# Optimization experiments

Hardware: AMD Instinct MI355X
Metric: run time of the kernel (lower is better)

Reference implementation:

```python
import jax, jax.numpy as jnp
import numpy as np

N = 50000   # nodes
E = 640000  # edges
IN = 256    # in_dim
H = 128     # hidden
OUT = 40    # out_dim
EPS = 1e-5  # BatchNorm eps


def setup_inputs() -> dict:
    key = jax.random.key(0)
    ks = jax.random.split(key, 14)
    x = jax.random.normal(ks[0], (N, IN), jnp.float32)
    edge_index = jax.random.randint(ks[1], (2, E), 0, N)
    def lin(k, fan_in, shape):
        return jax.random.normal(k, shape, jnp.float32) / np.float32(np.sqrt(fan_in))
    return {
        "x": x,
        "edge_index": edge_index,
        # block 0 (256 -> 128, has res_proj)
        "W0": lin(ks[2], IN, (IN, H)),
        "b0": jnp.zeros((H,), jnp.float32),
        "g0": jnp.ones((H,), jnp.float32),
        "be0": jnp.zeros((H,), jnp.float32),
        "pW": lin(ks[3], IN, (IN, H)),
        "pb": jnp.zeros((H,), jnp.float32),
        # block 1 (128 -> 128, identity residual)
        "W1": lin(ks[4], H, (H, H)),
        "b1": jnp.zeros((H,), jnp.float32),
        "g1": jnp.ones((H,), jnp.float32),
        "be1": jnp.zeros((H,), jnp.float32),
        # head
        "hW": lin(ks[5], H, (H, OUT)),
        "hb": jnp.zeros((OUT,), jnp.float32),
    }


def _gcn_conv(x, W, b, edge_index):
    """GCNConv(improved=True): x' = D^-1/2 (A + 2I) D^-1/2 (x W) + b."""
    h = x @ W  # [N, dout]
    row, col = edge_index[0], edge_index[1]  # source -> target
    # degree of A + 2I (edge_weight = 1, self-loop fill = 2.0)
    deg = jnp.zeros((N,), h.dtype).at[col].add(1.0) + 2.0
    dis = jax.lax.rsqrt(deg)  # deg > 0 always (self-loops)
    norm = dis[row] * dis[col]  # [E]
    # neighbor aggregation: scatter-add normalized messages to targets
    agg = jnp.zeros_like(h).at[col].add(norm[:, None] * h[row])
    # self-loop contribution with weight 2.0
    agg = agg + (2.0 * dis * dis)[:, None] * h
    return agg + b


def _bn(x, gamma, beta):
    # batch statistics (training-mode BatchNorm math), biased variance
    m = jnp.mean(x, axis=0)
    v = jnp.mean(jnp.square(x - m), axis=0)
    return (x - m) * jax.lax.rsqrt(v + EPS) * gamma + beta


def reference(x, edge_index, W0, b0, g0, be0, pW, pb, W1, b1, g1, be1, hW, hb):
    # block 0: conv -> bn -> relu -> (+ res_proj(x))
    out = jax.nn.relu(_bn(_gcn_conv(x, W0, b0, edge_index), g0, be0))
    x1 = out + (x @ pW + pb)
    # block 1: conv -> bn -> relu -> (+ identity)
    out = jax.nn.relu(_bn(_gcn_conv(x1, W1, b1, edge_index), g1, be1))
    x2 = out + x1
    return x2 @ hW + hb  # [N, OUT]
```

## Files before the change

kernel.cpp:

```cpp
#include <hip/hip_runtime.h>

#define H 128
#define IN_DIM 256
#define OUT_DIM 40
#define EPS 1e-5f

typedef unsigned short ushortT;
typedef __attribute__((ext_vector_type(8))) short bf16x8;
typedef __attribute__((ext_vector_type(4))) float f32x4;

static __device__ __forceinline__ ushortT f2bf(float f) {
    union { float f; unsigned u; } v; v.f = f;
    unsigned r = v.u + 0x7FFF + ((v.u >> 16) & 1);
    return (ushortT)(r >> 16);
}
static __device__ __forceinline__ unsigned pk2(float a, float b) {
    return (unsigned)f2bf(a) | ((unsigned)f2bf(b) << 16);
}
static __device__ __forceinline__ float bflo(unsigned v) {
    union { unsigned u; float f; } t; t.u = v << 16; return t.f;
}
static __device__ __forceinline__ float bfhi(unsigned v) {
    union { unsigned u; float f; } t; t.u = v & 0xFFFF0000u; return t.f;
}


__global__ __launch_bounds__(256) void count_kernel(const int* __restrict__ ei, int E, int* __restrict__ cnt) {
    int e = blockIdx.x * 256 + threadIdx.x;
    if (e < E) atomicAdd(&cnt[ei[E + e]], 1);
}

__global__ __launch_bounds__(256) void scan_block_sum(const int* __restrict__ cnt, int* __restrict__ bsum,
                                                      float* __restrict__ dis, int N) {
    __shared__ int s[256];
    int i = blockIdx.x * 256 + threadIdx.x;
    int v = (i < N) ? cnt[i] : 0;
    if (i < N) dis[i] = rsqrtf((float)v + 2.0f);
    s[threadIdx.x] = v;
    __syncthreads();
    for (int o = 128; o > 0; o >>= 1) {
        if (threadIdx.x < o) s[threadIdx.x] += s[threadIdx.x + o];
        __syncthreads();
    }
    if (threadIdx.x == 0) bsum[blockIdx.x] = s[0];
}

__global__ void scan_tops(const int* __restrict__ bsum, int* __restrict__ boff, int* __restrict__ rowptrN, int nb) {
    __shared__ int s[256];
    int t = threadIdx.x;
    int v = (t < nb) ? bsum[t] : 0;
    s[t] = v;
    __syncthreads();
    for (int o = 1; o < 256; o <<= 1) {
        int u = (t >= o) ? s[t - o] : 0;
        __syncthreads();
        s[t] += u;
        __syncthreads();
    }
    if (t < nb) boff[t] = s[t] - v;
    if (t == 255) *rowptrN = s[255];
}

__global__ __launch_bounds__(256) void scan_final(const int* __restrict__ cnt, const int* __restrict__ boff,
                                                  int* __restrict__ rowptr, int* __restrict__ cursor, int N) {
    __shared__ int s[256];
    int t = threadIdx.x;
    int i = blockIdx.x * 256 + t;
    int v = (i < N) ? cnt[i] : 0;
    s[t] = v;
    __syncthreads();
    for (int o = 1; o < 256; o <<= 1) {
        int u = (t >= o) ? s[t - o] : 0;
        __syncthreads();
        s[t] += u;
        __syncthreads();
    }
    if (i < N) {
        int e = boff[blockIdx.x] + s[t] - v;
        rowptr[i] = e;
        cursor[i] = e;
    }
}

__global__ __launch_bounds__(256) void fill_xcd(const int* __restrict__ ei, int E, int nper,
                                                int* __restrict__ cursor, int* __restrict__ eidx) {
    int xcd = blockIdx.x & 7;
    int nchunk = gridDim.x >> 3;
    int chunk = blockIdx.x >> 3;
    int csz = (E + nchunk - 1) / nchunk;
    int beg = chunk * csz;
    int end = min(E, beg + csz);
    for (int e = beg + (int)threadIdx.x; e < end; e += 256) {
        int c = ei[E + e];
        if (c / nper == xcd) {
            int slot = atomicAdd(&cursor[c], 1);
            eidx[slot] = ei[e];
        }
    }
}


__global__ __launch_bounds__(256) void prep_weights(const float* __restrict__ W0, const float* __restrict__ pW,
                                                    const float* __restrict__ W1, const float* __restrict__ hW,
                                                    ushortT* __restrict__ Wt0, ushortT* __restrict__ WtP,
                                                    ushortT* __restrict__ Wt1, ushortT* __restrict__ WtH) {
    int i = blockIdx.x * 256 + threadIdx.x;
    if (i < 32768) { int n = i >> 8, k = i & 255; Wt0[i] = f2bf(W0[k * 128 + n]); WtP[i] = f2bf(pW[k * 128 + n]); }
    if (i < 16384) { int n = i >> 7, k = i & 127; Wt1[i] = f2bf(W1[k * 128 + n]); }
    if (i < 6144)  { int n = i >> 7, k = i & 127; WtH[i] = (n < OUT_DIM) ? f2bf(hW[k * OUT_DIM + n]) : (ushortT)0; }
}


__global__ __launch_bounds__(512) void mgemm0(const float* __restrict__ X,
                                              const ushortT* __restrict__ Wt0,
                                              const ushortT* __restrict__ WtP,
                                              const float* __restrict__ pb,
                                              ushortT* __restrict__ Oh,
                                              ushortT* __restrict__ Op,
                                              int N) {
    __shared__ __align__(16) ushortT As[64][264];
    int tid = threadIdx.x;
    int brow = blockIdx.x * 64;

#pragma unroll
    for (int i = 0; i < 8; ++i) {
        int idx = i * 512 + tid;
        int row = idx >> 6, c4 = idx & 63;
        int gr = brow + row;
        float4 v = make_float4(0.f, 0.f, 0.f, 0.f);
        if (gr < N) v = *(const float4*)&X[(size_t)gr * IN_DIM + c4 * 4];
        uint2 p;
        p.x = pk2(v.x, v.y);
        p.y = pk2(v.z, v.w);
        *(uint2*)&As[row][c4 * 4] = p;
    }
    __syncthreads();

    int w = tid >> 6, lane = tid & 63;
    int lm = lane & 15, lk = lane >> 4;
    int mat = w >> 2;
    int colbase = (w & 3) * 32;
    const ushortT* Wt = mat ? WtP : Wt0;

    f32x4 acc[4][2];
#pragma unroll
    for (int mt = 0; mt < 4; ++mt)
#pragma unroll
        for (int nt = 0; nt < 2; ++nt) acc[mt][nt] = (f32x4)0.f;

#pragma unroll
    for (int kc = 0; kc < 2; ++kc) {
        bf16x8 breg[2][4];
#pragma unroll
        for (int nt = 0; nt < 2; ++nt)
#pragma unroll
            for (int ks = 0; ks < 4; ++ks)
                breg[nt][ks] = *(const bf16x8*)&Wt[(size_t)(colbase + nt * 16 + lm) * IN_DIM + kc * 128 + ks * 32 + lk * 8];
#pragma unroll
        for (int ks = 0; ks < 4; ++ks) {
            bf16x8 af[4];
#pragma unroll
            for (int mt = 0; mt < 4; ++mt)
                af[mt] = *(const bf16x8*)&As[mt * 16 + lm][kc * 128 + ks * 32 + lk * 8];
#pragma unroll
            for (int nt = 0; nt < 2; ++nt)
#pragma unroll
                for (int mt = 0; mt < 4; ++mt)
                    acc[mt][nt] = __builtin_amdgcn_mfma_f32_16x16x32_bf16(af[mt], breg[nt][ks], acc[mt][nt], 0, 0, 0);
        }
    }

    float bb[2] = {0.f, 0.f};
    if (mat) {
        bb[0] = pb[colbase + lm];
        bb[1] = pb[colbase + 16 + lm];
    }
    ushortT* O = mat ? Op : Oh;
#pragma unroll
    for (int mt = 0; mt < 4; ++mt)
#pragma unroll
        for (int nt = 0; nt < 2; ++nt) {
            int col = colbase + nt * 16 + lm;
#pragma unroll
            for (int j = 0; j < 4; ++j) {
                int r = brow + mt * 16 + lk * 4 + j;
                if (r < N) O[(size_t)r * 128 + col] = f2bf(acc[mt][nt][j] + bb[nt]);
            }
        }
}


__global__ __launch_bounds__(512) void mgemm1(const ushortT* __restrict__ Xb,
                                              const ushortT* __restrict__ Wt1,
                                              ushortT* __restrict__ O,
                                              int N) {
    __shared__ __align__(16) ushortT As[128][136];
    int tid = threadIdx.x;
    int brow = blockIdx.x * 128;

#pragma unroll
    for (int i = 0; i < 4; ++i) {
        int idx = i * 512 + tid;
        int row = idx >> 4, q = idx & 15;
        int gr = brow + row;
        uint4 v = make_uint4(0u, 0u, 0u, 0u);
        if (gr < N) v = *(const uint4*)&Xb[(size_t)gr * H + q * 8];
        *(uint4*)&As[row][q * 8] = v;
    }
    __syncthreads();

    int w = tid >> 6, lane = tid & 63;
    int lm = lane & 15, lk = lane >> 4;
    int rh = (w >> 2) * 64;
    int colbase = (w & 3) * 32;

    bf16x8 breg[2][4];
#pragma unroll
    for (int nt = 0; nt < 2; ++nt)
#pragma unroll
        for (int ks = 0; ks < 4; ++ks)
            breg[nt][ks] = *(const bf16x8*)&Wt1[(size_t)(colbase + nt * 16 + lm) * H + ks * 32 + lk * 8];

    f32x4 acc[4][2];
#pragma unroll
    for (int mt = 0; mt < 4; ++mt)
#pragma unroll
        for (int nt = 0; nt < 2; ++nt) acc[mt][nt] = (f32x4)0.f;

#pragma unroll
    for (int ks = 0; ks < 4; ++ks) {
        bf16x8 af[4];
#pragma unroll
        for (int mt = 0; mt < 4; ++mt)
            af[mt] = *(const bf16x8*)&As[rh + mt * 16 + lm][ks * 32 + lk * 8];
#pragma unroll
        for (int nt = 0; nt < 2; ++nt)
#pragma unroll
            for (int mt = 0; mt < 4; ++mt)
                acc[mt][nt] = __builtin_amdgcn_mfma_f32_16x16x32_bf16(af[mt], breg[nt][ks], acc[mt][nt], 0, 0, 0);
    }

#pragma unroll
    for (int mt = 0; mt < 4; ++mt)
#pragma unroll
        for (int nt = 0; nt < 2; ++nt) {
            int col = colbase + nt * 16 + lm;
#pragma unroll
            for (int j = 0; j < 4; ++j) {
                int r = brow + rh + mt * 16 + lk * 4 + j;
                if (r < N) O[(size_t)r * 128 + col] = f2bf(acc[mt][nt][j]);
            }
        }
}


__global__ __launch_bounds__(256) void aggregate_bf(const ushortT* __restrict__ h,
                                                    const int* __restrict__ rowptr,
                                                    const int* __restrict__ eidx,
                                                    const float* __restrict__ dis,
                                                    ushortT* __restrict__ aggb, int N) {
    int n = blockIdx.x * 4 + (threadIdx.x >> 6);
    int lane = threadIdx.x & 63;
    if (n >= N) return;
    int beg = rowptr[n], end = rowptr[n + 1];
    float dn = dis[n];
    const unsigned* h1 = (const unsigned*)h;
    float a0x = 0.f, a0y = 0.f, a1x = 0.f, a1y = 0.f;
    float a2x = 0.f, a2y = 0.f, a3x = 0.f, a3y = 0.f;
    int p = beg;
    for (; p + 3 < end; p += 4) {
        int s0 = eidx[p], s1 = eidx[p + 1], s2 = eidx[p + 2], s3 = eidx[p + 3];
        float n0 = dis[s0] * dn, n1 = dis[s1] * dn, n2 = dis[s2] * dn, n3 = dis[s3] * dn;
        unsigned v0 = h1[(size_t)s0 * 64 + lane];
        unsigned v1 = h1[(size_t)s1 * 64 + lane];
        unsigned v2 = h1[(size_t)s2 * 64 + lane];
        unsigned v3 = h1[(size_t)s3 * 64 + lane];
        a0x = fmaf(n0, bflo(v0), a0x); a0y = fmaf(n0, bfhi(v0), a0y);
        a1x = fmaf(n1, bflo(v1), a1x); a1y = fmaf(n1, bfhi(v1), a1y);
        a2x = fmaf(n2, bflo(v2), a2x); a2y = fmaf(n2, bfhi(v2), a2y);
        a3x = fmaf(n3, bflo(v3), a3x); a3y = fmaf(n3, bfhi(v3), a3y);
    }
    for (; p < end; ++p) {
        int s0 = eidx[p];
        float n0 = dis[s0] * dn;
        unsigned v0 = h1[(size_t)s0 * 64 + lane];
        a0x = fmaf(n0, bflo(v0), a0x); a0y = fmaf(n0, bfhi(v0), a0y);
    }
    {
        unsigned v = h1[(size_t)n * 64 + lane];
        float sw = 2.f * dn * dn;
        a0x = fmaf(sw, bflo(v), a0x); a0y = fmaf(sw, bfhi(v), a0y);
    }
    float rx = (a0x + a1x) + (a2x + a3x);
    float ry = (a0y + a1y) + (a2y + a3y);
    ((unsigned*)aggb)[(size_t)n * 64 + lane] = pk2(rx, ry);
}


__global__ __launch_bounds__(256) void stats_bf(const unsigned* __restrict__ v, int totalU,
                                                float* __restrict__ sums) {
    int tid = blockIdx.x * 256 + threadIdx.x;
    int stride = gridDim.x * 256;
    float sx = 0.f, sy = 0.f, qx = 0.f, qy = 0.f;
    for (int i = tid; i < totalU; i += stride) {
        unsigned u = v[i];
        float a = bflo(u), b = bfhi(u);
        sx += a; sy += b;
        qx = fmaf(a, a, qx); qy = fmaf(b, b, qy);
    }
    __shared__ float l0[256], l1[256], l2[256], l3[256];
    int t = threadIdx.x;
    l0[t] = sx; l1[t] = sy; l2[t] = qx; l3[t] = qy;
    __syncthreads();
    if (t < 64) {
        sx = (l0[t] + l0[t + 64]) + (l0[t + 128] + l0[t + 192]);
        sy = (l1[t] + l1[t + 64]) + (l1[t + 128] + l1[t + 192]);
        qx = (l2[t] + l2[t + 64]) + (l2[t + 128] + l2[t + 192]);
        qy = (l3[t] + l3[t + 64]) + (l3[t + 128] + l3[t + 192]);
        atomicAdd(&sums[2 * t], sx);
        atomicAdd(&sums[2 * t + 1], sy);
        atomicAdd(&sums[128 + 2 * t], qx);
        atomicAdd(&sums[128 + 2 * t + 1], qy);
    }
}


__global__ __launch_bounds__(256) void bn_relu_add_v3(const uint2* __restrict__ aggb,
                                                      const float* __restrict__ stats,
                                                      const float* __restrict__ g,
                                                      const float* __restrict__ be,
                                                      const uint2* __restrict__ projb,
                                                      uint2* __restrict__ x1b, int N) {
    __shared__ float sc[128], sh[128];
    int t = threadIdx.x;
    if (t < 128) {
        float mean = stats[t] / (float)N;
        float var = stats[128 + t] / (float)N - mean * mean;
        float inv = rsqrtf(var + EPS);
        float s = g[t] * inv;
        sc[t] = s;
        sh[t] = be[t] - mean * s;
    }
    __syncthreads();
    size_t i2 = (size_t)blockIdx.x * 256 + t;
    size_t total2 = (size_t)N * 32;
    if (i2 >= total2) return;
    int ch = (int)(i2 & 31) * 4;
    uint2 a = aggb[i2];
    uint2 d = projb[i2];
    float v0 = fmaxf(fmaf(bflo(a.x), sc[ch + 0], sh[ch + 0]), 0.f) + bflo(d.x);
    float v1 = fmaxf(fmaf(bfhi(a.x), sc[ch + 1], sh[ch + 1]), 0.f) + bfhi(d.x);
    float v2 = fmaxf(fmaf(bflo(a.y), sc[ch + 2], sh[ch + 2]), 0.f) + bflo(d.y);
    float v3 = fmaxf(fmaf(bfhi(a.y), sc[ch + 3], sh[ch + 3]), 0.f) + bfhi(d.y);
    uint2 r;
    r.x = pk2(v0, v1);
    r.y = pk2(v2, v3);
    x1b[i2] = r;
}


__global__ __launch_bounds__(256) void head_fused(const uint4* __restrict__ aggb,
                                                  const uint4* __restrict__ x1b,
                                                  const float* __restrict__ stats,
                                                  const float* __restrict__ g,
                                                  const float* __restrict__ be,
                                                  const ushortT* __restrict__ WtH,
                                                  const float* __restrict__ hb,
                                                  float* __restrict__ out, int N) {
    __shared__ __align__(16) ushortT As[64][136];
    __shared__ __align__(16) ushortT Bs[48][136];
    __shared__ float sc[128], sh[128];

    int tid = threadIdx.x;
    int brow = blockIdx.x * 64;
    int w = tid >> 6, lane = tid & 63;
    int lm = lane & 15, lk = lane >> 4;

    if (tid < 128) {
        float mean = stats[tid] / (float)N;
        float var = stats[128 + tid] / (float)N - mean * mean;
        float inv = rsqrtf(var + EPS);
        float s = g[tid] * inv;
        sc[tid] = s;
        sh[tid] = be[tid] - mean * s;
    }
    if (tid < 192) {
        int row = tid >> 2, q = tid & 3;
        const uint4* src = (const uint4*)&WtH[(size_t)row * H + q * 32];
        uint4 a = src[0], b = src[1], c = src[2], d = src[3];
        uint4* dst = (uint4*)&Bs[row][q * 32];
        dst[0] = a; dst[1] = b; dst[2] = c; dst[3] = d;
    }
    __syncthreads();
#pragma unroll
    for (int k = 0; k < 4; ++k) {
        int idx = k * 256 + tid;
        int row = idx >> 4, colq = idx & 15;
        int gr = brow + row;
        uint4 a = make_uint4(0u, 0u, 0u, 0u), x = a;
        if (gr < N) {
            size_t gidx = (size_t)brow * 16 + idx;
            a = aggb[gidx];
            x = x1b[gidx];
        }
        int ch = colq * 8;
        float v0 = fmaxf(fmaf(bflo(a.x), sc[ch + 0], sh[ch + 0]), 0.f) + bflo(x.x);
        float v1 = fmaxf(fmaf(bfhi(a.x), sc[ch + 1], sh[ch + 1]), 0.f) + bfhi(x.x);
        float v2 = fmaxf(fmaf(bflo(a.y), sc[ch + 2], sh[ch + 2]), 0.f) + bflo(x.y);
        float v3 = fmaxf(fmaf(bfhi(a.y), sc[ch + 3], sh[ch + 3]), 0.f) + bfhi(x.y);
        float v4 = fmaxf(fmaf(bflo(a.z), sc[ch + 4], sh[ch + 4]), 0.f) + bflo(x.z);
        float v5 = fmaxf(fmaf(bfhi(a.z), sc[ch + 5], sh[ch + 5]), 0.f) + bfhi(x.z);
        float v6 = fmaxf(fmaf(bflo(a.w), sc[ch + 6], sh[ch + 6]), 0.f) + bflo(x.w);
        float v7 = fmaxf(fmaf(bfhi(a.w), sc[ch + 7], sh[ch + 7]), 0.f) + bfhi(x.w);
        uint4 pv;
        pv.x = pk2(v0, v1);
        pv.y = pk2(v2, v3);
        pv.z = pk2(v4, v5);
        pv.w = pk2(v6, v7);
        *(uint4*)&As[row][colq * 8] = pv;
    }
    __syncthreads();

    f32x4 acc[3];
#pragma unroll
    for (int nt = 0; nt < 3; ++nt) acc[nt] = (f32x4)0.f;
#pragma unroll
    for (int ks = 0; ks < 4; ++ks) {
        bf16x8 a = *(const bf16x8*)&As[w * 16 + lm][ks * 32 + lk * 8];
#pragma unroll
        for (int nt = 0; nt < 3; ++nt) {
            bf16x8 b = *(const bf16x8*)&Bs[nt * 16 + lm][ks * 32 + lk * 8];
            acc[nt] = __builtin_amdgcn_mfma_f32_16x16x32_bf16(a, b, acc[nt], 0, 0, 0);
        }
    }
#pragma unroll
    for (int nt = 0; nt < 3; ++nt) {
        int col = nt * 16 + lm;
        if (col < OUT_DIM) {
            float bbv = hb[col];
#pragma unroll
            for (int j = 0; j < 4; ++j) {
                int r = brow + w * 16 + lk * 4 + j;
                if (r < N) out[(size_t)r * OUT_DIM + col] = acc[nt][j] + bbv;
            }
        }
    }
}


extern "C" void kernel_launch(void* const* d_in, const int* in_sizes, int n_in,
                              void* d_out, int out_size, void* d_ws, size_t ws_size,
                              hipStream_t stream) {
    const float* x   = (const float*)d_in[0];
    const int*   ei  = (const int*)d_in[1];
    const float* W0  = (const float*)d_in[2];
    const float* g0  = (const float*)d_in[4];
    const float* be0 = (const float*)d_in[5];
    const float* pW  = (const float*)d_in[6];
    const float* pb  = (const float*)d_in[7];
    const float* W1  = (const float*)d_in[8];
    const float* g1  = (const float*)d_in[10];
    const float* be1 = (const float*)d_in[11];
    const float* hW  = (const float*)d_in[12];
    const float* hb  = (const float*)d_in[13];
    float* out = (float*)d_out;

    int N = in_sizes[0] / IN_DIM;
    int E = in_sizes[1] / 2;
    size_t NH = (size_t)N * H;

    ushortT* hb16   = (ushortT*)d_ws;
    ushortT* aggb   = hb16 + NH;
    ushortT* projb  = aggb + NH;
    ushortT* x1b    = projb + NH;
    float*   dis    = (float*)(x1b + NH);
    int*     cnt    = (int*)(dis + N);
    int*     rowptr = cnt + N;
    int*     cursor = rowptr + (N + 1);
    int*     eidx   = cursor + N;
    float*   stats  = (float*)(eidx + E);
    ushortT* Wt0    = (ushortT*)(stats + 256);
    ushortT* WtP    = Wt0 + 128 * 256;
    ushortT* Wt1    = WtP + 128 * 256;
    ushortT* WtH    = Wt1 + 128 * 128;
    int*     bsum   = (int*)(WtH + 48 * 128);
    int*     boff   = bsum + 256;

    int gE = (E + 255) / 256;
    int nb = (N + 255) / 256;
    int g64 = (N + 63) / 64;
    int g128 = (N + 127) / 128;
    int gAgg = (N + 3) / 4;
    int gNH2 = (int)((NH / 4 + 255) / 256);

    hipMemsetAsync(cnt, 0, (size_t)N * sizeof(int), stream);
    prep_weights<<<128, 256, 0, stream>>>(W0, pW, W1, hW, Wt0, WtP, Wt1, WtH);
    count_kernel<<<gE, 256, 0, stream>>>(ei, E, cnt);
    scan_block_sum<<<nb, 256, 0, stream>>>(cnt, bsum, dis, N);
    scan_tops<<<1, 256, 0, stream>>>(bsum, boff, &rowptr[N], nb);
    scan_final<<<nb, 256, 0, stream>>>(cnt, boff, rowptr, cursor, N);
    fill_xcd<<<2048, 256, 0, stream>>>(ei, E, (N + 7) / 8, cursor, eidx);

    mgemm0<<<g64, 512, 0, stream>>>(x, Wt0, WtP, pb, hb16, projb, N);
    aggregate_bf<<<gAgg, 256, 0, stream>>>(hb16, rowptr, eidx, dis, aggb, N);
    hipMemsetAsync(stats, 0, 256 * sizeof(float), stream);
    stats_bf<<<256, 256, 0, stream>>>((const unsigned*)aggb, (int)(NH / 2), stats);
    bn_relu_add_v3<<<gNH2, 256, 0, stream>>>((const uint2*)aggb, stats, g0, be0,
                                             (const uint2*)projb, (uint2*)x1b, N);

    mgemm1<<<g128, 512, 0, stream>>>(x1b, Wt1, hb16, N);
    aggregate_bf<<<gAgg, 256, 0, stream>>>(hb16, rowptr, eidx, dis, aggb, N);
    hipMemsetAsync(stats, 0, 256 * sizeof(float), stream);
    stats_bf<<<256, 256, 0, stream>>>((const unsigned*)aggb, (int)(NH / 2), stats);

    head_fused<<<g64, 256, 0, stream>>>((const uint4*)aggb, (const uint4*)x1b, stats, g1, be1,
                                        WtH, hb, out, N);
}
```

Before: 274.2 us.

## Fuse BN-ReLU-residual into second GEMM and stage GEMM outputs through LDS

Removes the standalone BN/ReLU/residual kernel. The second GEMM now applies the batch-norm scale and shift, ReLU and projection add while loading its A tile, and writes x1 out as a side product. This saves one kernel launch and one extra read of the x1 tensor. Both GEMMs also stage their bf16 outputs in shared memory so the global stores become coalesced 16-byte writes instead of scattered 2-byte writes, at the cost of extra barriers and a larger LDS footprint.

Result: faster. 262.3 us (-4.3%).

```diff
diff --git a/kernel.cpp b/kernel.cpp
--- a/kernel.cpp
+++ b/kernel.cpp
@@ -118,7 +118,7 @@
                                               ushortT* __restrict__ Oh,
                                               ushortT* __restrict__ Op,
                                               int N) {
-    __shared__ __align__(16) ushortT As[64][264];
+    __shared__ __align__(16) ushortT S[17408];
     int tid = threadIdx.x;
     int brow = blockIdx.x * 64;
 
@@ -132,7 +132,7 @@
         uint2 p;
         p.x = pk2(v.x, v.y);
         p.y = pk2(v.z, v.w);
-        *(uint2*)&As[row][c4 * 4] = p;
+        *(uint2*)&S[row * 264 + c4 * 4] = p;
     }
     __syncthreads();
 
@@ -161,7 +161,7 @@
             bf16x8 af[4];
 #pragma unroll
             for (int mt = 0; mt < 4; ++mt)
-                af[mt] = *(const bf16x8*)&As[mt * 16 + lm][kc * 128 + ks * 32 + lk * 8];
+                af[mt] = *(const bf16x8*)&S[(mt * 16 + lm) * 264 + kc * 128 + ks * 32 + lk * 8];
 #pragma unroll
             for (int nt = 0; nt < 2; ++nt)
 #pragma unroll
@@ -175,7 +175,7 @@
         bb[0] = pb[colbase + lm];
         bb[1] = pb[colbase + 16 + lm];
     }
-    ushortT* O = mat ? Op : Oh;
+    __syncthreads();
 #pragma unroll
     for (int mt = 0; mt < 4; ++mt)
 #pragma unroll
@@ -183,29 +183,78 @@
             int col = colbase + nt * 16 + lm;
 #pragma unroll
             for (int j = 0; j < 4; ++j) {
-                int r = brow + mt * 16 + lk * 4 + j;
-                if (r < N) O[(size_t)r * 128 + col] = f2bf(acc[mt][nt][j] + bb[nt]);
+                int row = mt * 16 + lk * 4 + j;
+                S[mat * 8704 + row * 136 + col] = f2bf(acc[mt][nt][j] + bb[nt]);
             }
         }
-}
-
-
-__global__ __launch_bounds__(512) void mgemm1(const ushortT* __restrict__ Xb,
-                                              const ushortT* __restrict__ Wt1,
-                                              ushortT* __restrict__ O,
-                                              int N) {
-    __shared__ __align__(16) ushortT As[128][136];
+    __syncthreads();
+#pragma unroll
+    for (int i = 0; i < 4; ++i) {
+        int idx = i * 512 + tid;
+        int m2 = idx >> 10;
+        int rem = idx & 1023;
+        int row = rem >> 4, colq = rem & 15;
+        int gr = brow + row;
+        if (gr < N) {
+            uint4 v = *(const uint4*)&S[m2 * 8704 + row * 136 + colq * 8];
+            ushortT* O = m2 ? Op : Oh;
+            *(uint4*)&O[(size_t)gr * 128 + colq * 8] = v;
+        }
+    }
+}
+
+
+__global__ __launch_bounds__(512) void mgemm1_fused(const uint4* __restrict__ aggb,
+                                                    const uint4* __restrict__ projb,
+                                                    const float* __restrict__ stats,
+                                                    const float* __restrict__ g,
+                                                    const float* __restrict__ be,
+                                                    const ushortT* __restrict__ Wt1,
+                                                    ushortT* __restrict__ O,
+                                                    uint4* __restrict__ x1b,
+                                                    int N) {
+    __shared__ __align__(16) ushortT S[17408];
+    __shared__ float sc[128], sh[128];
     int tid = threadIdx.x;
     int brow = blockIdx.x * 128;
+
+    if (tid < 128) {
+        float mean = stats[tid] / (float)N;
+        float var = stats[128 + tid] / (float)N - mean * mean;
+        float inv = rsqrtf(var + EPS);
+        float s = g[tid] * inv;
+        sc[tid] = s;
+        sh[tid] = be[tid] - mean * s;
+    }
+    __syncthreads();
 
 #pragma unroll
     for (int i = 0; i < 4; ++i) {
         int idx = i * 512 + tid;
         int row = idx >> 4, q = idx & 15;
         int gr = brow + row;
-        uint4 v = make_uint4(0u, 0u, 0u, 0u);
-        if (gr < N) v = *(const uint4*)&Xb[(size_t)gr * H + q * 8];
-        *(uint4*)&As[row][q * 8] = v;
+        uint4 a = make_uint4(0u, 0u, 0u, 0u), p = a;
+        if (gr < N) {
+            size_t gidx = (size_t)gr * 16 + q;
+            a = aggb[gidx];
+            p = projb[gidx];
+        }
+        int ch = q * 8;
+        float v0 = fmaxf(fmaf(bflo(a.x), sc[ch + 0], sh[ch + 0]), 0.f) + bflo(p.x);
+        float v1 = fmaxf(fmaf(bfhi(a.x), sc[ch + 1], sh[ch + 1]), 0.f) + bfhi(p.x);
+        float v2 = fmaxf(fmaf(bflo(a.y), sc[ch + 2], sh[ch + 2]), 0.f) + bflo(p.y);
+        float v3 = fmaxf(fmaf(bfhi(a.y), sc[ch + 3], sh[ch + 3]), 0.f) + bfhi(p.y);
+        float v4 = fmaxf(fmaf(bflo(a.z), sc[ch + 4], sh[ch + 4]), 0.f) + bflo(p.z);
+        float v5 = fmaxf(fmaf(bfhi(a.z), sc[ch + 5], sh[ch + 5]), 0.f) + bfhi(p.z);
+        float v6 = fmaxf(fmaf(bflo(a.w), sc[ch + 6], sh[ch + 6]), 0.f) + bflo(p.w);
+        float v7 = fmaxf(fmaf(bfhi(a.w), sc[ch + 7], sh[ch + 7]), 0.f) + bfhi(p.w);
+        uint4 pv;
+        pv.x = pk2(v0, v1);
+        pv.y = pk2(v2, v3);
+        pv.z = pk2(v4, v5);
+        pv.w = pk2(v6, v7);
+        *(uint4*)&S[row * 136 + q * 8] = pv;
+        if (gr < N) x1b[(size_t)gr * 16 + q] = pv;
     }
     __syncthreads();
 
@@ -232,7 +281,7 @@
         bf16x8 af[4];
 #pragma unroll
         for (int mt = 0; mt < 4; ++mt)
-            af[mt] = *(const bf16x8*)&As[rh + mt * 16 + lm][ks * 32 + lk * 8];
+            af[mt] = *(const bf16x8*)&S[(rh + mt * 16 + lm) * 136 + ks * 32 + lk * 8];
 #pragma unroll
         for (int nt = 0; nt < 2; ++nt)
 #pragma unroll
@@ -240,6 +289,7 @@
                 acc[mt][nt] = __builtin_amdgcn_mfma_f32_16x16x32_bf16(af[mt], breg[nt][ks], acc[mt][nt], 0, 0, 0);
     }
 
+    __syncthreads();
 #pragma unroll
     for (int mt = 0; mt < 4; ++mt)
 #pragma unroll
@@ -247,10 +297,21 @@
             int col = colbase + nt * 16 + lm;
 #pragma unroll
             for (int j = 0; j < 4; ++j) {
-                int r = brow + rh + mt * 16 + lk * 4 + j;
-                if (r < N) O[(size_t)r * 128 + col] = f2bf(acc[mt][nt][j]);
+                int row = rh + mt * 16 + lk * 4 + j;
+                S[row * 136 + col] = f2bf(acc[mt][nt][j]);
             }
         }
+    __syncthreads();
+#pragma unroll
+    for (int i = 0; i < 4; ++i) {
+        int idx = i * 512 + tid;
+        int row = idx >> 4, colq = idx & 15;
+        int gr = brow + row;
+        if (gr < N) {
+            uint4 v = *(const uint4*)&S[row * 136 + colq * 8];
+            *(uint4*)&O[(size_t)gr * 128 + colq * 8] = v;
+        }
+    }
 }
 
 
@@ -325,40 +386,6 @@
 }
 
 
-__global__ __launch_bounds__(256) void bn_relu_add_v3(const uint2* __restrict__ aggb,
-                                                      const float* __restrict__ stats,
-                                                      const float* __restrict__ g,
-                                                      const float* __restrict__ be,
-                                                      const uint2* __restrict__ projb,
-                                                      uint2* __restrict__ x1b, int N) {
-    __shared__ float sc[128], sh[128];
-    int t = threadIdx.x;
-    if (t < 128) {
-        float mean = stats[t] / (float)N;
-        float var = stats[128 + t] / (float)N - mean * mean;
-        float inv = rsqrtf(var + EPS);
-        float s = g[t] * inv;
-        sc[t] = s;
-        sh[t] = be[t] - mean * s;
-    }
-    __syncthreads();
-    size_t i2 = (size_t)blockIdx.x * 256 + t;
-    size_t total2 = (size_t)N * 32;
-    if (i2 >= total2) return;
-    int ch = (int)(i2 & 31) * 4;
-    uint2 a = aggb[i2];
-    uint2 d = projb[i2];
-    float v0 = fmaxf(fmaf(bflo(a.x), sc[ch + 0], sh[ch + 0]), 0.f) + bflo(d.x);
-    float v1 = fmaxf(fmaf(bfhi(a.x), sc[ch + 1], sh[ch + 1]), 0.f) + bfhi(d.x);
-    float v2 = fmaxf(fmaf(bflo(a.y), sc[ch + 2], sh[ch + 2]), 0.f) + bflo(d.y);
-    float v3 = fmaxf(fmaf(bfhi(a.y), sc[ch + 3], sh[ch + 3]), 0.f) + bfhi(d.y);
-    uint2 r;
-    r.x = pk2(v0, v1);
-    r.y = pk2(v2, v3);
-    x1b[i2] = r;
-}
-
-
 __global__ __launch_bounds__(256) void head_fused(const uint4* __restrict__ aggb,
                                                   const uint4* __restrict__ x1b,
                                                   const float* __restrict__ stats,
@@ -491,7 +518,6 @@
     int g64 = (N + 63) / 64;
     int g128 = (N + 127) / 128;
     int gAgg = (N + 3) / 4;
-    int gNH2 = (int)((NH / 4 + 255) / 256);
 
     hipMemsetAsync(cnt, 0, (size_t)N * sizeof(int), stream);
     prep_weights<<<128, 256, 0, stream>>>(W0, pW, W1, hW, Wt0, WtP, Wt1, WtH);
@@ -505,10 +531,9 @@
     aggregate_bf<<<gAgg, 256, 0, stream>>>(hb16, rowptr, eidx, dis, aggb, N);
     hipMemsetAsync(stats, 0, 256 * sizeof(float), stream);
     stats_bf<<<256, 256, 0, stream>>>((const unsigned*)aggb, (int)(NH / 2), stats);
-    bn_relu_add_v3<<<gNH2, 256, 0, stream>>>((const uint2*)aggb, stats, g0, be0,
-                                             (const uint2*)projb, (uint2*)x1b, N);
-
-    mgemm1<<<g128, 512, 0, stream>>>(x1b, Wt1, hb16, N);
+
+    mgemm1_fused<<<g128, 512, 0, stream>>>((const uint4*)aggb, (const uint4*)projb, stats, g0, be0,
+                                           Wt1, hb16, (uint4*)x1b, N);
     aggregate_bf<<<gAgg, 256, 0, stream>>>(hb16, rowptr, eidx, dis, aggb, N);
     hipMemsetAsync(stats, 0, 256 * sizeof(float), stream);
     stats_bf<<<256, 256, 0, stream>>>((const unsigned*)aggb, (int)(NH / 2), stats);
```
